# Optimization experiments

Hardware: AMD Instinct MI355X
Metric: run time of the kernel (lower is better)

## Reference

```python
import jax, jax.numpy as jnp
import numpy as np

B, H, S, D = 2, 16, 2048, 64


def setup_inputs() -> dict:
    key = jax.random.key(0)
    k1, k2, k3, k4 = jax.random.split(key, 4)
    Hin = jax.random.normal(k1, (B, H, S, D), dtype=jnp.float32)
    Hk = jax.random.normal(k2, (B, H, S, D), dtype=jnp.float32)
    Hv = jax.random.normal(k3, (B, H, S, D), dtype=jnp.float32)
    # causal lookahead mask: 1 above diagonal (disallowed), 0 elsewhere
    mask = jnp.triu(jnp.ones((S, S), dtype=jnp.float32), k=1)[None, None, :, :]
    # per-head learned G_LM cache matrix avAp: [H, D, D]
    avAp = jax.random.normal(k4, (H, D, D), dtype=jnp.float32) * (1.0 / np.sqrt(D))
    return {"Hin": Hin, "Hk": Hk, "Hv": Hv, "mask": mask, "avAp": avAp, "F_hidden": D}


def reference(Hin, Hk, Hv, mask, avAp, F_hidden):
    # WHiWHj = Hin @ avAp  : [B,H,S,D] x [H,D,D] -> [B,H,S,D]
    WHiWHj = jnp.einsum("bhsd,hde->bhse", Hin, avAp)
    # Ep = WHiWHj @ Hk^T / sqrt(dk) : [B,H,S,S]
    scale = 1.0 / jnp.sqrt(jnp.float32(F_hidden))
    Ep = jnp.einsum("bhse,bhte->bhst", WHiWHj, Hk) * scale
    E = jax.nn.softmax(Ep + mask * (-1e9), axis=-1)
    # Hout = E @ Hv : [B,H,S,D]
    return jnp.einsum("bhst,bhtd->bhsd", E, Hv)
```

## Files before the change

### kernel.cpp

```cpp
#include <hip/hip_runtime.h>

#define S_LEN 2048
#define NBH 32

typedef unsigned short u16;
typedef unsigned int u32;
typedef __attribute__((ext_vector_type(8))) short bf16x8;
typedef __attribute__((ext_vector_type(4))) float f32x4;

#define MFMA16(A, B, C) __builtin_amdgcn_mfma_f32_16x16x32_bf16(A, B, C, 0, 0, 0)

__device__ __forceinline__ u16 f2bf(float f) {
  u32 u = __builtin_bit_cast(u32, f);
  u += 0x7fffu + ((u >> 16) & 1u);
  return (u16)(u >> 16);
}
__device__ __forceinline__ float bf2f(u16 b) {
  u32 u = ((u32)b) << 16;
  return __builtin_bit_cast(float, u);
}
__device__ __forceinline__ u32 pack2(float a, float b) {
  return (u32)f2bf(a) | ((u32)f2bf(b) << 16);
}

__global__ __launch_bounds__(256, 2) void vtprep_kernel(
    const float* __restrict__ Hv, u16* __restrict__ Vt) {
  __shared__ u16 sT[64 * 66];
  const int bh = blockIdx.y, s0 = blockIdx.x * 64, tid = threadIdx.x;
  const size_t base = ((size_t)bh * S_LEN + s0) * 64;

#pragma unroll
  for (int i = 0; i < 2; ++i) {
    int c = tid + 256 * i;
    int row = c >> 3, col8 = (c & 7) * 8;
    const float* src = Hv + base + (size_t)row * 64 + col8;
    float4 a = *(const float4*)src;
    float4 b = *(const float4*)(src + 4);
    u16* dst = sT + row * 66 + col8;
    *(u32*)(dst + 0) = pack2(a.x, a.y);
    *(u32*)(dst + 2) = pack2(a.z, a.w);
    *(u32*)(dst + 4) = pack2(b.x, b.y);
    *(u32*)(dst + 6) = pack2(b.z, b.w);
  }
  __syncthreads();

#pragma unroll
  for (int i = 0; i < 2; ++i) {
    int c = tid + 256 * i;
    int d = c >> 3, s8 = (c & 7) * 8;
    u16 tmp[8];
#pragma unroll
    for (int j = 0; j < 8; ++j) tmp[j] = sT[(s8 + j) * 66 + d];
    *(uint4*)(Vt + ((size_t)bh * 64 + d) * S_LEN + s0 + s8) = *(uint4*)tmp;
  }
}

__global__ __launch_bounds__(512, 4) void attn_kernel(
    const float* __restrict__ Hin, const float* __restrict__ avAp,
    const float* __restrict__ Hk, const u16* __restrict__ Vt,
    float* __restrict__ Out) {
  __shared__ __align__(16) char smem[65536];

  const int bh = blockIdx.y;
  const int h = bh & 15;
  const int x = blockIdx.x;
  const int qtile = ((bh >> 4) & 1) ? x : (15 - x);
  const int q0 = qtile * 128;
  const int tid = threadIdx.x, wave = tid >> 6, lane = tid & 63;
  const int lr = lane & 15, lg = lane >> 4;
  const int qrow = q0 + wave * 16 + lr;
  const int nT = 2 * qtile + 2;

  const int srow = tid >> 3, sc16 = tid & 7;
  const int sdst = srow * 128 + ((sc16 * 16) ^ ((srow & 7) << 4));
  const float* kgp = Hk + ((size_t)bh * S_LEN + srow) * 64 + sc16 * 8;
  const u16* vgp = Vt + ((size_t)bh * 64 + srow) * S_LEN + sc16 * 8;

  float4 kaP = *(const float4*)(kgp);
  float4 kbP = *(const float4*)(kgp + 4);
  bf16x8 rvP = *(const bf16x8*)(vgp);

  float* sA = (float*)(smem + 49152);
#pragma unroll
  for (int i = 0; i < 2; ++i) {
    int c = tid + 512 * i;
    *(float4*)(sA + c * 4) = *(const float4*)(avAp + (size_t)h * 4096 + c * 4);
  }

  bf16x8 ahi[2], alo[2];
#pragma unroll
  for (int kk = 0; kk < 2; ++kk) {
    const float* src =
        Hin + ((size_t)bh * S_LEN + qrow) * 64 + kk * 32 + lg * 8;
    float4 u = *(const float4*)src;
    float4 w = *(const float4*)(src + 4);
    float xs[8] = {u.x, u.y, u.z, u.w, w.x, w.y, w.z, w.w};
#pragma unroll
    for (int j = 0; j < 8; ++j) {
      u16 hh = f2bf(xs[j]);
      ahi[kk][j] = (short)hh;
      alo[kk][j] = (short)f2bf(xs[j] - bf2f(hh));
    }
  }
  __syncthreads();

  f32x4 qa[4];
#pragma unroll
  for (int nb = 0; nb < 4; ++nb) qa[nb] = (f32x4){0.f, 0.f, 0.f, 0.f};
#pragma unroll
  for (int kk = 0; kk < 2; ++kk) {
    bf16x8 bhiK[4], bloK[4];
#pragma unroll
    for (int nb = 0; nb < 4; ++nb) {
#pragma unroll
      for (int j = 0; j < 8; ++j) {
        float xv = sA[(kk * 32 + lg * 8 + j) * 64 + nb * 16 + lr];
        u16 hh = f2bf(xv);
        bhiK[nb][j] = (short)hh;
        bloK[nb][j] = (short)f2bf(xv - bf2f(hh));
      }
    }
#pragma unroll
    for (int nb = 0; nb < 4; ++nb) {
      qa[nb] = MFMA16(bhiK[nb], ahi[kk], qa[nb]);
      qa[nb] = MFMA16(bloK[nb], ahi[kk], qa[nb]);
      qa[nb] = MFMA16(bhiK[nb], alo[kk], qa[nb]);
    }
  }
  __syncthreads();

  const float QSCALE = 0.125f * 1.44269504088896f;
  char* sPw = smem + 49152 + wave * 2048;
  bf16x8 qhi[2], qlo[2];
#pragma unroll
  for (int nb = 0; nb < 4; ++nb)
#pragma unroll
    for (int i = 0; i < 2; ++i) {
      int e = nb * 16 + lg * 4 + 2 * i;
      *(u32*)(sPw + lr * 128 + ((e * 2) ^ ((lr & 7) << 4))) =
          pack2(qa[nb][2 * i] * QSCALE, qa[nb][2 * i + 1] * QSCALE);
    }
#pragma unroll
  for (int kk = 0; kk < 2; ++kk)
    qhi[kk] = *(const bf16x8*)(sPw + lr * 128 +
                               ((kk * 64 + lg * 16) ^ ((lr & 7) << 4)));
#pragma unroll
  for (int nb = 0; nb < 4; ++nb)
#pragma unroll
    for (int i = 0; i < 2; ++i) {
      int e = nb * 16 + lg * 4 + 2 * i;
      float v0 = qa[nb][2 * i] * QSCALE, v1 = qa[nb][2 * i + 1] * QSCALE;
      *(u32*)(sPw + lr * 128 + ((e * 2) ^ ((lr & 7) << 4))) =
          pack2(v0 - bf2f(f2bf(v0)), v1 - bf2f(f2bf(v1)));
    }
#pragma unroll
  for (int kk = 0; kk < 2; ++kk)
    qlo[kk] = *(const bf16x8*)(sPw + lr * 128 +
                               ((kk * 64 + lg * 16) ^ ((lr & 7) << 4)));

  int buf = 0;
  {
    float xs[8] = {kaP.x, kaP.y, kaP.z, kaP.w, kbP.x, kbP.y, kbP.z, kbP.w};
    bf16x8 khi8, klo8;
#pragma unroll
    for (int j = 0; j < 8; ++j) {
      u16 hh = f2bf(xs[j]);
      khi8[j] = (short)hh;
      klo8[j] = (short)f2bf(xs[j] - bf2f(hh));
    }
    *(bf16x8*)(smem + sdst) = khi8;
    *(bf16x8*)(smem + 16384 + sdst) = klo8;
    *(bf16x8*)(smem + 32768 + sdst) = rvP;
  }
  __syncthreads();

  f32x4 Oacc[4];
#pragma unroll
  for (int db = 0; db < 4; ++db) Oacc[db] = (f32x4){0.f, 0.f, 0.f, 0.f};
  float m_r = -3.0e38f, l_r = 0.f;

  for (int t = 0; t < nT; ++t) {
    const int kv0 = t * 64;
    const bool pf = (t + 1 < nT);
    if (pf) {
      const size_t ko = (size_t)(kv0 + 64) * 64;
      kaP = *(const float4*)(kgp + ko);
      kbP = *(const float4*)(kgp + ko + 4);
      rvP = *(const bf16x8*)(vgp + kv0 + 64);
    }

    const int bK = buf * 8192;
    if (kv0 <= q0 + wave * 16 + 15) {
      f32x4 sacc[4];
#pragma unroll
      for (int nb = 0; nb < 4; ++nb) sacc[nb] = (f32x4){0.f, 0.f, 0.f, 0.f};
#pragma unroll
      for (int nb = 0; nb < 4; ++nb) {
        int krow = nb * 16 + lr;
#pragma unroll
        for (int kk = 0; kk < 2; ++kk) {
          int off = krow * 128 + ((kk * 64 + lg * 16) ^ ((krow & 7) << 4));
          bf16x8 kh = *(const bf16x8*)(smem + bK + off);
          bf16x8 kl = *(const bf16x8*)(smem + 16384 + bK + off);
          sacc[nb] = MFMA16(kh, qhi[kk], sacc[nb]);
          sacc[nb] = MFMA16(kl, qhi[kk], sacc[nb]);
          sacc[nb] = MFMA16(kh, qlo[kk], sacc[nb]);
        }
      }

      if (kv0 + 63 > q0 + wave * 16) {
#pragma unroll
        for (int nb = 0; nb < 4; ++nb)
#pragma unroll
          for (int r = 0; r < 4; ++r)
            if (kv0 + nb * 16 + lg * 4 + r > qrow) sacc[nb][r] = -1.0e30f;
      }

      float tmax = sacc[0][0];
#pragma unroll
      for (int nb = 0; nb < 4; ++nb)
#pragma unroll
        for (int r = 0; r < 4; ++r) tmax = fmaxf(tmax, sacc[nb][r]);
      tmax = fmaxf(tmax, __shfl_xor(tmax, 16));
      tmax = fmaxf(tmax, __shfl_xor(tmax, 32));
      float mn = fmaxf(m_r, tmax);
      float corr = exp2f(m_r - mn);
      m_r = mn;
      float rs = 0.f;
#pragma unroll
      for (int nb = 0; nb < 4; ++nb)
#pragma unroll
        for (int r = 0; r < 4; ++r) {
          float e = exp2f(sacc[nb][r] - mn);
          sacc[nb][r] = e;
          rs += e;
        }
      rs += __shfl_xor(rs, 16);
      rs += __shfl_xor(rs, 32);
      l_r = l_r * corr + rs;
#pragma unroll
      for (int db = 0; db < 4; ++db) Oacc[db] *= corr;

#pragma unroll
      for (int nb = 0; nb < 4; ++nb)
#pragma unroll
        for (int i = 0; i < 2; ++i) {
          int kv = nb * 16 + lg * 4 + 2 * i;
          *(u32*)(sPw + lr * 128 + ((kv * 2) ^ ((lr & 7) << 4))) =
              pack2(sacc[nb][2 * i], sacc[nb][2 * i + 1]);
        }
      bf16x8 pa[2];
#pragma unroll
      for (int kk = 0; kk < 2; ++kk)
        pa[kk] = *(const bf16x8*)(sPw + lr * 128 +
                                  ((kk * 64 + lg * 16) ^ ((lr & 7) << 4)));

#pragma unroll
      for (int db = 0; db < 4; ++db) {
        int vrow = db * 16 + lr;
#pragma unroll
        for (int kk = 0; kk < 2; ++kk) {
          int off = vrow * 128 + ((kk * 64 + lg * 16) ^ ((vrow & 7) << 4));
          bf16x8 vb = *(const bf16x8*)(smem + 32768 + bK + off);
          Oacc[db] = MFMA16(vb, pa[kk], Oacc[db]);
        }
      }
    }

    if (pf) {
      const int bN = (buf ^ 1) * 8192;
      float xs[8] = {kaP.x, kaP.y, kaP.z, kaP.w, kbP.x, kbP.y, kbP.z, kbP.w};
      bf16x8 khi8, klo8;
#pragma unroll
      for (int j = 0; j < 8; ++j) {
        u16 hh = f2bf(xs[j]);
        khi8[j] = (short)hh;
        klo8[j] = (short)f2bf(xs[j] - bf2f(hh));
      }
      *(bf16x8*)(smem + bN + sdst) = khi8;
      *(bf16x8*)(smem + 16384 + bN + sdst) = klo8;
      *(bf16x8*)(smem + 32768 + bN + sdst) = rvP;
    }
    __syncthreads();
    buf ^= 1;
  }

  float invl = 1.0f / l_r;
  float* orow = Out + ((size_t)bh * S_LEN + qrow) * 64;
#pragma unroll
  for (int db = 0; db < 4; ++db) {
    float4 o = make_float4(Oacc[db][0] * invl, Oacc[db][1] * invl,
                           Oacc[db][2] * invl, Oacc[db][3] * invl);
    *(float4*)(orow + db * 16 + lg * 4) = o;
  }
}

extern "C" void kernel_launch(void* const* d_in, const int* in_sizes, int n_in,
                              void* d_out, int out_size, void* d_ws,
                              size_t ws_size, hipStream_t stream) {
  const float* Hin = (const float*)d_in[0];
  const float* Hk = (const float*)d_in[1];
  const float* Hv = (const float*)d_in[2];
  const float* avAp = (const float*)d_in[4];
  float* Out = (float*)d_out;

  u16* Vt = (u16*)d_ws;

  vtprep_kernel<<<dim3(S_LEN / 64, NBH), dim3(256), 0, stream>>>(Hv, Vt);
  attn_kernel<<<dim3(S_LEN / 128, NBH), dim3(512), 0, stream>>>(Hin, avAp, Hk,
                                                                Vt, Out);
}
```

Baseline: 170.9 us.

## Pre-split K into bf16 hi/lo tiles in prep kernel and stream via global_load_lds

The prep kernel now converts K into pre-swizzled bf16 hi/lo tiles and lays out V-transpose in per-tile blocks. The attention kernel loads each tile straight into LDS with global_load_lds instead of staging through registers and converting on every reuse. It also skips the online-softmax rescale when the running max grows by no more than 8, uses v_cvt_pk_bf16_f32 to pack P, and swizzles the avAp LDS layout. The cost is extra workspace and prep traffic, and the lazy rescale assumes exp2 of up to 8 stays safe in fp32.

Measured after the change: 161.8 us. 1.06x faster.

```diff
diff --git a/kernel.cpp b/kernel.cpp
--- a/kernel.cpp
+++ b/kernel.cpp
@@ -22,43 +22,67 @@
 __device__ __forceinline__ u32 pack2(float a, float b) {
   return (u32)f2bf(a) | ((u32)f2bf(b) << 16);
 }
-
-__global__ __launch_bounds__(256, 2) void vtprep_kernel(
-    const float* __restrict__ Hv, u16* __restrict__ Vt) {
+__device__ __forceinline__ u32 cvtpk(float a, float b) {
+  u32 r;
+  asm("v_cvt_pk_bf16_f32 %0, %1, %2" : "=v"(r) : "v"(a), "v"(b));
+  return r;
+}
+__device__ __forceinline__ void gld16(const void* g, void* l) {
+  __builtin_amdgcn_global_load_lds(
+      (const __attribute__((address_space(1))) void*)g,
+      (__attribute__((address_space(3))) void*)l, 16, 0, 0);
+}
+
+__global__ __launch_bounds__(256) void prep_kernel(
+    const float* __restrict__ Hk, const float* __restrict__ Hv,
+    u16* __restrict__ Khb, u16* __restrict__ Klb, u16* __restrict__ Vtb) {
   __shared__ u16 sT[64 * 66];
-  const int bh = blockIdx.y, s0 = blockIdx.x * 64, tid = threadIdx.x;
-  const size_t base = ((size_t)bh * S_LEN + s0) * 64;
+  const int bh = blockIdx.y, t = blockIdx.x, tid = threadIdx.x;
+  const size_t base = ((size_t)bh * S_LEN + t * 64) * 64;
+  const size_t bb = ((size_t)bh * 32 + t) * 4096;
 
 #pragma unroll
   for (int i = 0; i < 2; ++i) {
     int c = tid + 256 * i;
-    int row = c >> 3, col8 = (c & 7) * 8;
-    const float* src = Hv + base + (size_t)row * 64 + col8;
-    float4 a = *(const float4*)src;
-    float4 b = *(const float4*)(src + 4);
-    u16* dst = sT + row * 66 + col8;
-    *(u32*)(dst + 0) = pack2(a.x, a.y);
-    *(u32*)(dst + 2) = pack2(a.z, a.w);
-    *(u32*)(dst + 4) = pack2(b.x, b.y);
-    *(u32*)(dst + 6) = pack2(b.z, b.w);
+    int row = c >> 3, ci = c & 7;
+    const float* ks = Hk + base + (size_t)row * 64 + ci * 8;
+    float4 a = *(const float4*)ks, b = *(const float4*)(ks + 4);
+    float xs[8] = {a.x, a.y, a.z, a.w, b.x, b.y, b.z, b.w};
+    u16 hi[8], lo[8];
+#pragma unroll
+    for (int j = 0; j < 8; ++j) {
+      hi[j] = f2bf(xs[j]);
+      lo[j] = f2bf(xs[j] - bf2f(hi[j]));
+    }
+    int o = (c & ~7) | (ci ^ (row & 7));
+    *(uint4*)(Khb + bb + o * 8) = *(uint4*)hi;
+    *(uint4*)(Klb + bb + o * 8) = *(uint4*)lo;
+
+    const float* vs = Hv + base + (size_t)row * 64 + ci * 8;
+    float4 va = *(const float4*)vs, vb = *(const float4*)(vs + 4);
+    u16* dst = sT + row * 66 + ci * 8;
+    *(u32*)(dst + 0) = pack2(va.x, va.y);
+    *(u32*)(dst + 2) = pack2(va.z, va.w);
+    *(u32*)(dst + 4) = pack2(vb.x, vb.y);
+    *(u32*)(dst + 6) = pack2(vb.z, vb.w);
   }
   __syncthreads();
 
 #pragma unroll
   for (int i = 0; i < 2; ++i) {
-    int c = tid + 256 * i;
-    int d = c >> 3, s8 = (c & 7) * 8;
+    int o = tid + 256 * i;
+    int d = o >> 3, s8 = ((o & 7) ^ (d & 7)) * 8;
     u16 tmp[8];
 #pragma unroll
     for (int j = 0; j < 8; ++j) tmp[j] = sT[(s8 + j) * 66 + d];
-    *(uint4*)(Vt + ((size_t)bh * 64 + d) * S_LEN + s0 + s8) = *(uint4*)tmp;
+    *(uint4*)(Vtb + bb + o * 8) = *(uint4*)tmp;
   }
 }
 
 __global__ __launch_bounds__(512, 4) void attn_kernel(
     const float* __restrict__ Hin, const float* __restrict__ avAp,
-    const float* __restrict__ Hk, const u16* __restrict__ Vt,
-    float* __restrict__ Out) {
+    const u16* __restrict__ Khb, const u16* __restrict__ Klb,
+    const u16* __restrict__ Vtb, float* __restrict__ Out) {
   __shared__ __align__(16) char smem[65536];
 
   const int bh = blockIdx.y;
@@ -71,20 +95,25 @@
   const int qrow = q0 + wave * 16 + lr;
   const int nT = 2 * qtile + 2;
 
-  const int srow = tid >> 3, sc16 = tid & 7;
-  const int sdst = srow * 128 + ((sc16 * 16) ^ ((srow & 7) << 4));
-  const float* kgp = Hk + ((size_t)bh * S_LEN + srow) * 64 + sc16 * 8;
-  const u16* vgp = Vt + ((size_t)bh * 64 + srow) * S_LEN + sc16 * 8;
-
-  float4 kaP = *(const float4*)(kgp);
-  float4 kbP = *(const float4*)(kgp + 4);
-  bf16x8 rvP = *(const bf16x8*)(vgp);
-
-  float* sA = (float*)(smem + 49152);
+#define STAGE(tt, bN)                                              \
+  {                                                                \
+    const size_t go = (((size_t)bh * 32 + (tt)) * 512 + tid) * 16; \
+    char* lw = smem + (bN) + wave * 1024;                          \
+    gld16((const char*)Khb + go, lw);                              \
+    gld16((const char*)Klb + go, lw + 16384);                      \
+    gld16((const char*)Vtb + go, lw + 32768);                      \
+  }
+
+  STAGE(0, 0);
+
+  char* sAB = smem + 49152;
 #pragma unroll
   for (int i = 0; i < 2; ++i) {
     int c = tid + 512 * i;
-    *(float4*)(sA + c * 4) = *(const float4*)(avAp + (size_t)h * 4096 + c * 4);
+    int d = c >> 4, c4 = c & 15;
+    int key = (((d >> 3) & 1) << 4) | (((d >> 4) & 1) << 6);
+    *(float4*)(sAB + d * 256 + ((c4 * 16) ^ key)) =
+        *(const float4*)(avAp + (size_t)h * 4096 + c * 4);
   }
 
   bf16x8 ahi[2], alo[2];
@@ -104,6 +133,7 @@
   }
   __syncthreads();
 
+  const int keyA = ((lg & 1) << 4) | ((lg >> 1) << 6);
   f32x4 qa[4];
 #pragma unroll
   for (int nb = 0; nb < 4; ++nb) qa[nb] = (f32x4){0.f, 0.f, 0.f, 0.f};
@@ -114,7 +144,8 @@
     for (int nb = 0; nb < 4; ++nb) {
 #pragma unroll
       for (int j = 0; j < 8; ++j) {
-        float xv = sA[(kk * 32 + lg * 8 + j) * 64 + nb * 16 + lr];
+        float xv = *(const float*)(sAB + (kk * 32 + lg * 8 + j) * 256 +
+                                   (((nb * 16 + lr) * 4) ^ keyA));
         u16 hh = f2bf(xv);
         bhiK[nb][j] = (short)hh;
         bloK[nb][j] = (short)f2bf(xv - bf2f(hh));
@@ -133,63 +164,45 @@
   char* sPw = smem + 49152 + wave * 2048;
   bf16x8 qhi[2], qlo[2];
 #pragma unroll
-  for (int nb = 0; nb < 4; ++nb)
-#pragma unroll
-    for (int i = 0; i < 2; ++i) {
-      int e = nb * 16 + lg * 4 + 2 * i;
-      *(u32*)(sPw + lr * 128 + ((e * 2) ^ ((lr & 7) << 4))) =
-          pack2(qa[nb][2 * i] * QSCALE, qa[nb][2 * i + 1] * QSCALE);
-    }
+  for (int nb = 0; nb < 4; ++nb) {
+    uint2 w;
+    w.x = pack2(qa[nb][0] * QSCALE, qa[nb][1] * QSCALE);
+    w.y = pack2(qa[nb][2] * QSCALE, qa[nb][3] * QSCALE);
+    *(uint2*)(sPw + lr * 128 + ((nb * 32 + lg * 8) ^ ((lr & 7) << 4))) = w;
+  }
 #pragma unroll
   for (int kk = 0; kk < 2; ++kk)
     qhi[kk] = *(const bf16x8*)(sPw + lr * 128 +
                                ((kk * 64 + lg * 16) ^ ((lr & 7) << 4)));
 #pragma unroll
-  for (int nb = 0; nb < 4; ++nb)
-#pragma unroll
-    for (int i = 0; i < 2; ++i) {
-      int e = nb * 16 + lg * 4 + 2 * i;
-      float v0 = qa[nb][2 * i] * QSCALE, v1 = qa[nb][2 * i + 1] * QSCALE;
-      *(u32*)(sPw + lr * 128 + ((e * 2) ^ ((lr & 7) << 4))) =
-          pack2(v0 - bf2f(f2bf(v0)), v1 - bf2f(f2bf(v1)));
-    }
+  for (int nb = 0; nb < 4; ++nb) {
+    float v[4];
+#pragma unroll
+    for (int r = 0; r < 4; ++r) {
+      float s = qa[nb][r] * QSCALE;
+      v[r] = s - bf2f(f2bf(s));
+    }
+    uint2 w;
+    w.x = pack2(v[0], v[1]);
+    w.y = pack2(v[2], v[3]);
+    *(uint2*)(sPw + lr * 128 + ((nb * 32 + lg * 8) ^ ((lr & 7) << 4))) = w;
+  }
 #pragma unroll
   for (int kk = 0; kk < 2; ++kk)
     qlo[kk] = *(const bf16x8*)(sPw + lr * 128 +
                                ((kk * 64 + lg * 16) ^ ((lr & 7) << 4)));
 
-  int buf = 0;
-  {
-    float xs[8] = {kaP.x, kaP.y, kaP.z, kaP.w, kbP.x, kbP.y, kbP.z, kbP.w};
-    bf16x8 khi8, klo8;
-#pragma unroll
-    for (int j = 0; j < 8; ++j) {
-      u16 hh = f2bf(xs[j]);
-      khi8[j] = (short)hh;
-      klo8[j] = (short)f2bf(xs[j] - bf2f(hh));
-    }
-    *(bf16x8*)(smem + sdst) = khi8;
-    *(bf16x8*)(smem + 16384 + sdst) = klo8;
-    *(bf16x8*)(smem + 32768 + sdst) = rvP;
-  }
-  __syncthreads();
-
   f32x4 Oacc[4];
 #pragma unroll
   for (int db = 0; db < 4; ++db) Oacc[db] = (f32x4){0.f, 0.f, 0.f, 0.f};
   float m_r = -3.0e38f, l_r = 0.f;
+  int buf = 0;
 
   for (int t = 0; t < nT; ++t) {
+    if (t + 1 < nT) STAGE(t + 1, (buf ^ 1) * 8192);
+    const int bK = buf * 8192;
     const int kv0 = t * 64;
-    const bool pf = (t + 1 < nT);
-    if (pf) {
-      const size_t ko = (size_t)(kv0 + 64) * 64;
-      kaP = *(const float4*)(kgp + ko);
-      kbP = *(const float4*)(kgp + ko + 4);
-      rvP = *(const bf16x8*)(vgp + kv0 + 64);
-    }
-
-    const int bK = buf * 8192;
+
     if (kv0 <= q0 + wave * 16 + 15) {
       f32x4 sacc[4];
 #pragma unroll
@@ -223,32 +236,34 @@
         for (int r = 0; r < 4; ++r) tmax = fmaxf(tmax, sacc[nb][r]);
       tmax = fmaxf(tmax, __shfl_xor(tmax, 16));
       tmax = fmaxf(tmax, __shfl_xor(tmax, 32));
-      float mn = fmaxf(m_r, tmax);
-      float corr = exp2f(m_r - mn);
-      m_r = mn;
+      if (!__all(tmax <= m_r + 8.0f)) {
+        float mn = fmaxf(m_r, tmax);
+        float corr = exp2f(m_r - mn);
+        m_r = mn;
+        l_r *= corr;
+#pragma unroll
+        for (int db = 0; db < 4; ++db) Oacc[db] *= corr;
+      }
       float rs = 0.f;
 #pragma unroll
       for (int nb = 0; nb < 4; ++nb)
 #pragma unroll
         for (int r = 0; r < 4; ++r) {
-          float e = exp2f(sacc[nb][r] - mn);
+          float e = exp2f(sacc[nb][r] - m_r);
           sacc[nb][r] = e;
           rs += e;
         }
       rs += __shfl_xor(rs, 16);
       rs += __shfl_xor(rs, 32);
-      l_r = l_r * corr + rs;
-#pragma unroll
-      for (int db = 0; db < 4; ++db) Oacc[db] *= corr;
-
-#pragma unroll
-      for (int nb = 0; nb < 4; ++nb)
-#pragma unroll
-        for (int i = 0; i < 2; ++i) {
-          int kv = nb * 16 + lg * 4 + 2 * i;
-          *(u32*)(sPw + lr * 128 + ((kv * 2) ^ ((lr & 7) << 4))) =
-              pack2(sacc[nb][2 * i], sacc[nb][2 * i + 1]);
-        }
+      l_r += rs;
+
+#pragma unroll
+      for (int nb = 0; nb < 4; ++nb) {
+        uint2 w;
+        w.x = cvtpk(sacc[nb][0], sacc[nb][1]);
+        w.y = cvtpk(sacc[nb][2], sacc[nb][3]);
+        *(uint2*)(sPw + lr * 128 + ((nb * 32 + lg * 8) ^ ((lr & 7) << 4))) = w;
+      }
       bf16x8 pa[2];
 #pragma unroll
       for (int kk = 0; kk < 2; ++kk)
@@ -267,20 +282,6 @@
       }
     }
 
-    if (pf) {
-      const int bN = (buf ^ 1) * 8192;
-      float xs[8] = {kaP.x, kaP.y, kaP.z, kaP.w, kbP.x, kbP.y, kbP.z, kbP.w};
-      bf16x8 khi8, klo8;
-#pragma unroll
-      for (int j = 0; j < 8; ++j) {
-        u16 hh = f2bf(xs[j]);
-        khi8[j] = (short)hh;
-        klo8[j] = (short)f2bf(xs[j] - bf2f(hh));
-      }
-      *(bf16x8*)(smem + bN + sdst) = khi8;
-      *(bf16x8*)(smem + 16384 + bN + sdst) = klo8;
-      *(bf16x8*)(smem + 32768 + bN + sdst) = rvP;
-    }
     __syncthreads();
     buf ^= 1;
   }
@@ -293,6 +294,7 @@
                            Oacc[db][2] * invl, Oacc[db][3] * invl);
     *(float4*)(orow + db * 16 + lg * 4) = o;
   }
+#undef STAGE
 }
 
 extern "C" void kernel_launch(void* const* d_in, const int* in_sizes, int n_in,
@@ -304,9 +306,13 @@
   const float* avAp = (const float*)d_in[4];
   float* Out = (float*)d_out;
 
-  u16* Vt = (u16*)d_ws;
-
-  vtprep_kernel<<<dim3(S_LEN / 64, NBH), dim3(256), 0, stream>>>(Hv, Vt);
-  attn_kernel<<<dim3(S_LEN / 128, NBH), dim3(512), 0, stream>>>(Hin, avAp, Hk,
-                                                                Vt, Out);
-}
+  const size_t N = (size_t)NBH * S_LEN * 64;
+  u16* Khb = (u16*)d_ws;
+  u16* Klb = Khb + N;
+  u16* Vtb = Klb + N;
+
+  prep_kernel<<<dim3(S_LEN / 64, NBH), dim3(256), 0, stream>>>(Hk, Hv, Khb,
+                                                               Klb, Vtb);
+  attn_kernel<<<dim3(S_LEN / 128, NBH), dim3(512), 0, stream>>>(
+      Hin, avAp, Khb, Klb, Vtb, Out);
+}
```
